# Kernel tuning notes

Hardware: AMD Instinct MI355X
Metric: run time of the kernel (lower is better)

The kernel has to match this reference:

```python
import jax, jax.numpy as jnp
import numpy as np

B, S, H, V, T, L = 32, 128, 1024, 32000, 100, 4
SD = 0.02


def setup_inputs() -> dict:
    key = jax.random.key(0)
    ks = jax.random.split(key, 20)
    f = jnp.float32
    return {
        "encoder_outputs": jax.random.normal(ks[0], (B, S, H), f),
        "encoder_hidden": jax.random.normal(ks[1], (L, B, H), f),
        "target_tensor": jax.random.randint(ks[2], (B, T), 0, V, dtype=jnp.int32),
        "emb": jax.random.normal(ks[3], (V, H), f) * SD,
        "w_ih0": jax.random.normal(ks[4], (3 * H, 2 * H), f) * SD,
        "w_hh0": jax.random.normal(ks[5], (3 * H, H), f) * SD,
        "b_ih0": jnp.zeros((3 * H,), f),
        "b_hh0": jnp.zeros((3 * H,), f),
        "w_ih": jax.random.normal(ks[6], (L - 1, 3 * H, H), f) * SD,
        "w_hh": jax.random.normal(ks[7], (L - 1, 3 * H, H), f) * SD,
        "b_ih": jnp.zeros((L - 1, 3 * H), f),
        "b_hh": jnp.zeros((L - 1, 3 * H), f),
        "out_w": jax.random.normal(ks[8], (V, H), f) * SD,
        "out_b": jnp.zeros((V,), f),
        "l1_w": jax.random.normal(ks[9], (3, 2 * H), f) * SD,
        "l1_b": jnp.zeros((3,), f),
        "l2_w": jax.random.normal(ks[10], (1, 3), f) * SD,
        "l2_b": jnp.zeros((1,), f),
    }


def _gru_cell(x, h, w_ih, w_hh, b_ih, b_hh):
    # PyTorch GRUCell math
    gi = x @ w_ih.T + b_ih          # [B, 3H]
    gh = h @ w_hh.T + b_hh          # [B, 3H]
    i_r, i_z, i_n = jnp.split(gi, 3, axis=-1)
    h_r, h_z, h_n = jnp.split(gh, 3, axis=-1)
    r = jax.nn.sigmoid(i_r + h_r)
    z = jax.nn.sigmoid(i_z + h_z)
    n = jnp.tanh(i_n + r * h_n)
    return (1.0 - z) * n + z * h


def reference(encoder_outputs, encoder_hidden, target_tensor, emb,
              w_ih0, w_hh0, b_ih0, b_hh0, w_ih, w_hh, b_ih, b_hh,
              out_w, out_b, l1_w, l1_b, l2_w, l2_b):
    b, h = encoder_hidden.shape[1], encoder_hidden.shape[2]
    enc_h = encoder_hidden[0]  # [B, H] 'updated_encoder_hidden'
    # teacher forcing: step 0 uses input 0, step i uses target[:, i-1]
    inputs = jnp.concatenate(
        [jnp.zeros((b, 1), target_tensor.dtype), target_tensor[:, :T - 1]],
        axis=1).T  # [T, B]

    def step(hidden, inp_t):
        # a[:] = hidden[0][-1] -> broadcast last batch row of layer-0 hidden
        a = jnp.broadcast_to(hidden[0, -1], (b, h))
        enc = jnp.concatenate([a, enc_h], axis=1)          # [B, 2H]
        s = (enc @ l1_w.T + l1_b) @ l2_w.T + l2_b          # [B, 1]
        scores = jax.nn.softmax(s, axis=0)                 # softmax over batch dim
        C = jnp.sum(enc_h * scores, axis=0)                # [H]
        e = jax.nn.relu(emb[inp_t])                        # [B, H]
        x = jnp.concatenate([e, jnp.broadcast_to(C, (b, h))], axis=-1)  # [B, 2H]
        h0 = _gru_cell(x, hidden[0], w_ih0, w_hh0, b_ih0, b_hh0)
        hs = [h0]
        xl = h0
        for l in range(L - 1):
            hl = _gru_cell(xl, hidden[l + 1], w_ih[l], w_hh[l], b_ih[l], b_hh[l])
            hs.append(hl)
            xl = hl
        logits = xl @ out_w.T + out_b                      # [B, V]
        return jnp.stack(hs), (logits, scores)

    hidden_fin, (logits, scores) = jax.lax.scan(step, encoder_hidden, inputs)
    dec_out = jax.nn.log_softmax(jnp.transpose(logits, (1, 0, 2)), axis=-1)  # [B, T, V]
    return dec_out, hidden_fin, scores[-1]
```

## Files before the change

### kernel.cpp

```cpp
#include <hip/hip_runtime.h>
#include <hip/hip_bf16.h>
#include <math.h>

#define B_ 32
#define H_ 1024
#define V_ 32000
#define T_ 100
#define L_ 4
#define TB_ (T_*B_)
#define N3H (3*H_)
#define NBLK 224
#define L0BLK 32
#define FSTRIDE 16

typedef __attribute__((ext_vector_type(8))) short bf16x8;
typedef __attribute__((ext_vector_type(4))) float f32x4;
typedef __attribute__((ext_vector_type(4))) unsigned short u16x4;

__device__ inline unsigned short f2bf(float f) {
    union { float f; unsigned u; } v; v.f = f;
    unsigned r = v.u + 0x7fff + ((v.u >> 16) & 1);
    return (unsigned short)(r >> 16);
}
__device__ inline float bf2f(unsigned short u) {
    union { unsigned u; float f; } v; v.u = ((unsigned)u) << 16; return v.f;
}

__device__ inline bf16x8 ld_h16(const unsigned short* p) {
    union { unsigned long long u[2]; bf16x8 v; } r;
    r.u[0] = __hip_atomic_load((const unsigned long long*)p,
                               __ATOMIC_RELAXED, __HIP_MEMORY_SCOPE_AGENT);
    r.u[1] = __hip_atomic_load((const unsigned long long*)(p + 4),
                               __ATOMIC_RELAXED, __HIP_MEMORY_SCOPE_AGENT);
    return r.v;
}
__device__ inline void st_h2(unsigned short* p, unsigned short v) {
    __hip_atomic_store(p, v, __ATOMIC_RELAXED, __HIP_MEMORY_SCOPE_AGENT);
}

__device__ inline void gload_lds16(const unsigned short* g, unsigned short* lds)
{
    __builtin_amdgcn_global_load_lds(
        (const __attribute__((address_space(1))) void*)g,
        (__attribute__((address_space(3))) void*)lds, 16, 0, 0);
}

__global__ __launch_bounds__(256) void convbf_kernel(
    const float* __restrict__ src, unsigned short* __restrict__ dst, int n4)
{
    for (int i = blockIdx.x * 256 + threadIdx.x; i < n4; i += gridDim.x * 256) {
        float4 v = ((const float4*)src)[i];
        u16x4 o; o.x = f2bf(v.x); o.y = f2bf(v.y); o.z = f2bf(v.z); o.w = f2bf(v.w);
        ((u16x4*)dst)[i] = o;
    }
}

__global__ __launch_bounds__(256) void embed_bf_kernel(
    const int* __restrict__ target, const float* __restrict__ emb,
    unsigned short* __restrict__ Ebf)
{
    int bid = blockIdx.x;
    int t = bid >> 5, b = bid & 31;
    int tok = (t == 0) ? 0 : target[b * T_ + (t - 1)];
    float4 v = ((const float4*)(emb + (size_t)tok * H_))[threadIdx.x];
    u16x4 o;
    o.x = f2bf(fmaxf(v.x, 0.f)); o.y = f2bf(fmaxf(v.y, 0.f));
    o.z = f2bf(fmaxf(v.z, 0.f)); o.w = f2bf(fmaxf(v.w, 0.f));
    ((u16x4*)(Ebf + (size_t)bid * H_))[threadIdx.x] = o;
}

__global__ __launch_bounds__(256) void attn_pre_kernel(
    const float* __restrict__ enc_h, const float* __restrict__ l1_w,
    const float* __restrict__ l1_b, const float* __restrict__ l2_w,
    float* __restrict__ Cout, float* __restrict__ scores)
{
    __shared__ float L1h[96];
    __shared__ float sc[32];
    int tid = threadIdx.x, wv = tid >> 6, lane = tid & 63;
    for (int d = wv; d < 96; d += 4) {
        int b = d / 3, g = d - 3 * b;
        const float4* wp = (const float4*)(l1_w + (size_t)g * 2 * H_ + H_);
        const float4* ep = (const float4*)(enc_h + (size_t)b * H_);
        float s = 0.f;
        for (int q = lane; q < 256; q += 64) {
            float4 w4 = wp[q], e4 = ep[q];
            s += w4.x * e4.x + w4.y * e4.y + w4.z * e4.z + w4.w * e4.w;
        }
        for (int o = 32; o > 0; o >>= 1) s += __shfl_down(s, o);
        if (lane == 0) L1h[d] = s;
    }
    __syncthreads();
    if (tid < 32) {
        float cb = 0.f;
        for (int g = 0; g < 3; ++g) cb += l2_w[g] * (L1h[tid * 3 + g] + l1_b[g]);
        sc[tid] = cb;
    }
    __syncthreads();
    if (tid == 0) {
        float m = sc[0];
        for (int b = 1; b < 32; ++b) m = fmaxf(m, sc[b]);
        float s = 0.f;
        for (int b = 0; b < 32; ++b) { float e = expf(sc[b] - m); sc[b] = e; s += e; }
        float inv = 1.f / s;
        for (int b = 0; b < 32; ++b) { sc[b] *= inv; scores[b] = sc[b]; }
    }
    __syncthreads();
    float4 c = make_float4(0.f, 0.f, 0.f, 0.f);
    for (int b = 0; b < 32; ++b) {
        float4 e = ((const float4*)(enc_h + (size_t)b * H_))[tid];
        float ww = sc[b];
        c.x += ww * e.x; c.y += ww * e.y; c.z += ww * e.z; c.w += ww * e.w;
    }
    ((float4*)Cout)[tid] = c;
}

__global__ __launch_bounds__(256) void wcc_kernel(
    const float* __restrict__ w_ih0, const float* __restrict__ C,
    float* __restrict__ wcC)
{
    int row = blockIdx.x * 4 + (threadIdx.x >> 6);
    int lane = threadIdx.x & 63;
    const float4* wp = (const float4*)(w_ih0 + (size_t)row * 2 * H_ + H_);
    const float4* cp = (const float4*)C;
    float s = 0.f;
    for (int q = lane; q < 256; q += 64) {
        float4 w4 = wp[q], c4 = cp[q];
        s += w4.x * c4.x + w4.y * c4.y + w4.z * c4.z + w4.w * c4.w;
    }
    for (int o = 32; o > 0; o >>= 1) s += __shfl_down(s, o);
    if (lane == 0) wcC[row] = s;
}

__global__ __launch_bounds__(256) void gemm_staged(
    const unsigned short* __restrict__ A, int lda,
    const unsigned short* __restrict__ Bb,
    const float* __restrict__ bias, int M, int outMode,
    void* __restrict__ outp)
{
    __shared__ unsigned short Wt[128 * 64];
    __shared__ unsigned short Ht[128 * 64];

    const int tid = threadIdx.x, wv = tid >> 6, lane = tid & 63;
    const int rlo = lane & 15, khw = lane >> 4;
    const int rch = lane >> 3, slot = lane & 7;
    const int rowB = blockIdx.y * 128, colB = blockIdx.x * 128;
    const int wrow0 = rowB + (wv >> 1) * 64;
    const int wcol0 = colB + (wv & 1) * 64;
    const int rA = (wv >> 1) * 64, cA = (wv & 1) * 64;

    f32x4 acc[4][4];
    #pragma unroll
    for (int i = 0; i < 4; ++i)
        #pragma unroll
        for (int j = 0; j < 4; ++j) acc[i][j] = (f32x4){0.f, 0.f, 0.f, 0.f};

    for (int k0 = 0; k0 < H_; k0 += 64) {
        #pragma unroll
        for (int j = 0; j < 4; ++j) {
            int q = wv * 4 + j;
            int row = q * 8 + rch;
            int ss = slot ^ (row & 7);
            gload_lds16(A + (size_t)(rowB + row) * lda + k0 + ss * 8,
                        Wt + (size_t)q * 512);
            gload_lds16(Bb + (size_t)(colB + row) * H_ + k0 + ss * 8,
                        Ht + (size_t)q * 512);
        }
        __syncthreads();

        const char* WtB = (const char*)Wt;
        const char* HtB = (const char*)Ht;
        #pragma unroll
        for (int kk = 0; kk < 2; ++kk) {
            bf16x8 af[4], bfr[4];
            #pragma unroll
            for (int ri = 0; ri < 4; ++ri) {
                int row = rA + ri * 16 + rlo;
                int ch = (kk * 4 + khw) ^ (row & 7);
                af[ri] = *(const bf16x8*)(WtB + row * 128 + ch * 16);
            }
            #pragma unroll
            for (int ci = 0; ci < 4; ++ci) {
                int col = cA + ci * 16 + rlo;
                int ch = (kk * 4 + khw) ^ (col & 7);
                bfr[ci] = *(const bf16x8*)(HtB + col * 128 + ch * 16);
            }
            #pragma unroll
            for (int ri = 0; ri < 4; ++ri)
                #pragma unroll
                for (int ci = 0; ci < 4; ++ci)
                    acc[ri][ci] = __builtin_amdgcn_mfma_f32_16x16x32_bf16(
                        af[ri], bfr[ci], acc[ri][ci], 0, 0, 0);
        }
        __syncthreads();
    }

    int rowoff = (lane >> 4) * 4;
    #pragma unroll
    for (int ri = 0; ri < 4; ++ri) {
        int row = wrow0 + ri * 16 + rowoff;
        float4 bs = *(const float4*)(bias + row);
        #pragma unroll
        for (int ci = 0; ci < 4; ++ci) {
            int col = wcol0 + ci * 16 + rlo;
            float4 v;
            v.x = acc[ri][ci][0] + bs.x; v.y = acc[ri][ci][1] + bs.y;
            v.z = acc[ri][ci][2] + bs.z; v.w = acc[ri][ci][3] + bs.w;
            if (outMode == 1) {
                int tt = col >> 5, b = col & 31;
                *(float4*)((float*)outp + ((size_t)b * T_ + tt) * V_ + row) = v;
            } else {
                u16x4 o; o.x = f2bf(v.x); o.y = f2bf(v.y);
                o.z = f2bf(v.z); o.w = f2bf(v.w);
                *(u16x4*)((unsigned short*)outp + (size_t)col * M + row) = o;
            }
        }
    }
}

__global__ __launch_bounds__(256) void big_gemm_kernel(
    const void* __restrict__ Aptr, int lda, int abf,
    const unsigned short* __restrict__ Bb,
    const float* __restrict__ bias, int M, int outMode,
    void* __restrict__ outp)
{
    int tid = threadIdx.x, wv = tid >> 6, lane = tid & 63;
    int rlo = lane & 15, klane = (lane >> 4) * 8;
    int rowB = blockIdx.y * 128 + (wv >> 1) * 64;
    int colB = blockIdx.x * 128 + (wv & 1) * 64;
    const unsigned short* Ab = (const unsigned short*)Aptr;
    const float* Af = (const float*)Aptr;

    f32x4 acc[4][4];
    #pragma unroll
    for (int i = 0; i < 4; ++i)
        #pragma unroll
        for (int j = 0; j < 4; ++j) acc[i][j] = (f32x4){0.f, 0.f, 0.f, 0.f};

    for (int k0 = 0; k0 < H_; k0 += 32) {
        bf16x8 bfrag[4];
        #pragma unroll
        for (int ci = 0; ci < 4; ++ci) {
            int col = colB + ci * 16 + rlo;
            bfrag[ci] = *(const bf16x8*)(Bb + (size_t)col * H_ + k0 + klane);
        }
        #pragma unroll
        for (int ri = 0; ri < 4; ++ri) {
            int row = rowB + ri * 16 + rlo;
            bf16x8 af;
            if (abf) {
                af = *(const bf16x8*)(Ab + (size_t)row * lda + k0 + klane);
            } else {
                const float* ap = Af + (size_t)row * lda + k0 + klane;
                float4 x0 = *(const float4*)ap, x1 = *(const float4*)(ap + 4);
                af[0] = (short)f2bf(x0.x); af[1] = (short)f2bf(x0.y);
                af[2] = (short)f2bf(x0.z); af[3] = (short)f2bf(x0.w);
                af[4] = (short)f2bf(x1.x); af[5] = (short)f2bf(x1.y);
                af[6] = (short)f2bf(x1.z); af[7] = (short)f2bf(x1.w);
            }
            #pragma unroll
            for (int ci = 0; ci < 4; ++ci)
                acc[ri][ci] = __builtin_amdgcn_mfma_f32_16x16x32_bf16(
                    af, bfrag[ci], acc[ri][ci], 0, 0, 0);
        }
    }

    int rowoff = (lane >> 4) * 4;
    #pragma unroll
    for (int ri = 0; ri < 4; ++ri) {
        int row = rowB + ri * 16 + rowoff;
        float4 bs = *(const float4*)(bias + row);
        #pragma unroll
        for (int ci = 0; ci < 4; ++ci) {
            int col = colB + ci * 16 + rlo;
            float4 v;
            v.x = acc[ri][ci][0] + bs.x; v.y = acc[ri][ci][1] + bs.y;
            v.z = acc[ri][ci][2] + bs.z; v.w = acc[ri][ci][3] + bs.w;
            if (outMode == 1) {
                int tt = col >> 5, b = col & 31;
                *(float4*)((float*)outp + ((size_t)b * T_ + tt) * V_ + row) = v;
            } else {
                u16x4 o; o.x = f2bf(v.x); o.y = f2bf(v.y);
                o.z = f2bf(v.z); o.w = f2bf(v.w);
                *(u16x4*)((unsigned short*)outp + (size_t)col * M + row) = o;
            }
        }
    }
}

__device__ inline void grid_bar4(unsigned* flags, unsigned round)
{
    __syncthreads();
    if (threadIdx.x == 0) {
        asm volatile("s_waitcnt vmcnt(0)" ::: "memory");
        __hip_atomic_store(&flags[(size_t)blockIdx.x * FSTRIDE], round,
                           __ATOMIC_RELAXED, __HIP_MEMORY_SCOPE_AGENT);
    }
    int ok = (threadIdx.x >= NBLK) ? 1 : 0;
    while (true) {
        if (!ok)
            ok = (__hip_atomic_load(&flags[(size_t)threadIdx.x * FSTRIDE],
                                    __ATOMIC_RELAXED, __HIP_MEMORY_SCOPE_AGENT) >= round);
        if (__syncthreads_and(ok)) break;
        __builtin_amdgcn_s_sleep(2);
    }
}

__global__ __launch_bounds__(512, 2) void decode_kernel(
    const unsigned short* __restrict__ whh0_bf,
    const unsigned short* __restrict__ wih_bf,
    const unsigned short* __restrict__ whh_bf,
    const unsigned short* __restrict__ G0,
    const float* __restrict__ b_ih0, const float* __restrict__ b_hh0,
    const float* __restrict__ b_ih,  const float* __restrict__ b_hh,
    const float* __restrict__ enc_hidden,
    unsigned short* __restrict__ hbf,
    unsigned short* __restrict__ Hist,
    float* __restrict__ hid_out,
    unsigned* __restrict__ flags)
{
    __shared__ float sacc[6][4][16][34];
    const int tid = threadIdx.x;
    const int wv = tid >> 6, lane = tid & 63;
    const int rlo = lane & 15, klane = (lane >> 4) * 8;
    const int rowoff = (lane >> 4) * 4;
    const int bid = blockIdx.x;

    int layer, f0;
    if (bid < L0BLK) { layer = 0; f0 = bid << 5; }
    else { int r = bid - L0BLK; layer = 1 + (r >> 6); f0 = (r & 63) << 4; }

    const unsigned short* Wih_l = (layer >= 1) ? wih_bf + (size_t)(layer - 1) * N3H * H_ : nullptr;
    const unsigned short* Whh_l = (layer >= 1) ? whh_bf + (size_t)(layer - 1) * N3H * H_ : whh0_bf;

    const int kc = wv & 3, srcgrp = wv >> 2;

    bf16x8 wreg[3][8];
    int rgv[3];
    #pragma unroll
    for (int i = 0; i < 3; ++i) {
        int rg = srcgrp * 3 + i;
        rgv[i] = rg;
        int wrow; const unsigned short* Wm;
        if (layer == 0)      { wrow = (rg >> 1) * H_ + f0 + (rg & 1) * 16; Wm = Whh_l; }
        else if (rg < 3)     { wrow = rg * H_ + f0;        Wm = Wih_l; }
        else                 { wrow = (rg - 3) * H_ + f0;  Wm = Whh_l; }
        const unsigned short* p = Wm + (size_t)(wrow + rlo) * H_ + kc * 256 + klane;
        #pragma unroll
        for (int s = 0; s < 8; ++s) wreg[i][s] = *(const bf16x8*)(p + s * 32);
    }

    const float* bihp = (layer == 0) ? b_ih0 : b_ih + (size_t)(layer - 1) * N3H;
    const float* bhhp = (layer == 0) ? b_hh0 : b_hh + (size_t)(layer - 1) * N3H;
    int jj, eb0;
    float hold0, hold1 = 0.f;
    if (layer == 0) {
        jj = f0 + (tid & 31);
        eb0 = tid >> 5;
        hold0 = enc_hidden[(size_t)eb0 * H_ + jj];
        hold1 = enc_hidden[(size_t)(eb0 + 16) * H_ + jj];
    } else {
        jj = f0 + (tid & 15);
        eb0 = tid >> 4;
        hold0 = enc_hidden[(size_t)layer * B_ * H_ + (size_t)eb0 * H_ + jj];
    }
    const float bir = bihp[jj], biz = bihp[H_ + jj], bin_ = bihp[2 * H_ + jj];
    const float bhr = bhhp[jj], bhz = bhhp[H_ + jj], bhn = bhhp[2 * H_ + jj];

    const size_t BH = (size_t)B_ * H_;

    for (int c = 0; c < T_ + L_ - 1; ++c) {
        int t = c - layer;
        if (t >= 0 && t < T_) {
            int pw = t & 1, pr = pw ^ 1;
            const unsigned short* hown  = hbf + ((size_t)pr * L_ + layer) * BH;
            const unsigned short* hprev = (layer > 0)
                ? hbf + ((size_t)pw * L_ + (layer - 1)) * BH : nullptr;

            f32x4 acc[3][2];
            #pragma unroll
            for (int i = 0; i < 3; ++i) {
                acc[i][0] = (f32x4){0.f, 0.f, 0.f, 0.f};
                acc[i][1] = (f32x4){0.f, 0.f, 0.f, 0.f};
            }

            const unsigned short* hsrc = (layer == 0 || srcgrp == 1) ? hown : hprev;
            const unsigned short* hp = hsrc + (size_t)rlo * H_ + kc * 256 + klane;
            #pragma unroll
            for (int s = 0; s < 8; ++s) {
                bf16x8 b0 = ld_h16(hp + s * 32);
                bf16x8 b1 = ld_h16(hp + 16 * H_ + s * 32);
                #pragma unroll
                for (int i = 0; i < 3; ++i) {
                    acc[i][0] = __builtin_amdgcn_mfma_f32_16x16x32_bf16(wreg[i][s], b0, acc[i][0], 0, 0, 0);
                    acc[i][1] = __builtin_amdgcn_mfma_f32_16x16x32_bf16(wreg[i][s], b1, acc[i][1], 0, 0, 0);
                }
            }

            #pragma unroll
            for (int i = 0; i < 3; ++i)
                #pragma unroll
                for (int r = 0; r < 4; ++r) {
                    sacc[rgv[i]][kc][rowoff + r][rlo]      = acc[i][0][r];
                    sacc[rgv[i]][kc][rowoff + r][16 + rlo] = acc[i][1][r];
                }
            __syncthreads();

            if (layer > 0) {
                int f = tid & 15, b = tid >> 4;
                float ir = bir, iz = biz, in_ = bin_;
                float hr = bhr, hz = bhz, hn = bhn;
                #pragma unroll
                for (int k2 = 0; k2 < 4; ++k2) {
                    ir += sacc[0][k2][f][b]; iz += sacc[1][k2][f][b]; in_ += sacc[2][k2][f][b];
                    hr += sacc[3][k2][f][b]; hz += sacc[4][k2][f][b]; hn += sacc[5][k2][f][b];
                }
                float r = 1.f / (1.f + expf(-(ir + hr)));
                float z = 1.f / (1.f + expf(-(iz + hz)));
                float n = tanhf(in_ + r * hn);
                float hnew = (1.f - z) * n + z * hold0;
                hold0 = hnew;
                unsigned short hb16 = f2bf(hnew);
                st_h2(&hbf[((size_t)pw * L_ + layer) * BH + (size_t)b * H_ + jj], hb16);
                if (layer == L_ - 1) Hist[((size_t)t * B_ + b) * H_ + jj] = hb16;
                if (t == T_ - 1) hid_out[(size_t)layer * BH + (size_t)b * H_ + jj] = hnew;
            } else {
                int fi = tid & 31;
                int rghalf = fi >> 4, fr = fi & 15;
                {
                    int b = eb0;
                    const unsigned short* g0p = G0 + ((size_t)t * B_ + b) * N3H;
                    float ir = bf2f(g0p[jj]) + bir;
                    float iz = bf2f(g0p[H_ + jj]) + biz;
                    float in_ = bf2f(g0p[2 * H_ + jj]) + bin_;
                    float hr = bhr, hz = bhz, hn = bhn;
                    #pragma unroll
                    for (int k2 = 0; k2 < 4; ++k2) {
                        hr += sacc[rghalf][k2][fr][b];
                        hz += sacc[2 + rghalf][k2][fr][b];
                        hn += sacc[4 + rghalf][k2][fr][b];
                    }
                    float r = 1.f / (1.f + expf(-(ir + hr)));
                    float z = 1.f / (1.f + expf(-(iz + hz)));
                    float n = tanhf(in_ + r * hn);
                    float hnew = (1.f - z) * n + z * hold0;
                    hold0 = hnew;
                    st_h2(&hbf[((size_t)pw * L_) * BH + (size_t)b * H_ + jj], f2bf(hnew));
                    if (t == T_ - 1) hid_out[(size_t)b * H_ + jj] = hnew;
                }
                {
                    int b = eb0 + 16;
                    const unsigned short* g0p = G0 + ((size_t)t * B_ + b) * N3H;
                    float ir = bf2f(g0p[jj]) + bir;
                    float iz = bf2f(g0p[H_ + jj]) + biz;
                    float in_ = bf2f(g0p[2 * H_ + jj]) + bin_;
                    float hr = bhr, hz = bhz, hn = bhn;
                    #pragma unroll
                    for (int k2 = 0; k2 < 4; ++k2) {
                        hr += sacc[rghalf][k2][fr][b];
                        hz += sacc[2 + rghalf][k2][fr][b];
                        hn += sacc[4 + rghalf][k2][fr][b];
                    }
                    float r = 1.f / (1.f + expf(-(ir + hr)));
                    float z = 1.f / (1.f + expf(-(iz + hz)));
                    float n = tanhf(in_ + r * hn);
                    float hnew = (1.f - z) * n + z * hold1;
                    hold1 = hnew;
                    st_h2(&hbf[((size_t)pw * L_) * BH + (size_t)b * H_ + jj], f2bf(hnew));
                    if (t == T_ - 1) hid_out[(size_t)b * H_ + jj] = hnew;
                }
            }
        }
        grid_bar4(flags, (unsigned)(c + 1));
    }
}

__global__ __launch_bounds__(256) void logsoftmax_kernel(float* __restrict__ dout)
{
    __shared__ float red[256];
    float4* x4 = (float4*)(dout + (size_t)blockIdx.x * V_);
    const int N4 = V_ / 4;
    int tid = threadIdx.x;

    float m = -INFINITY, s = 0.f;
    for (int i = tid; i < N4; i += 256) {
        float4 v = x4[i];
        float m4 = fmaxf(fmaxf(v.x, v.y), fmaxf(v.z, v.w));
        if (m4 > m) { s *= expf(m - m4); m = m4; }
        s += expf(v.x - m) + expf(v.y - m) + expf(v.z - m) + expf(v.w - m);
    }
    red[tid] = m; __syncthreads();
    for (int o = 128; o > 0; o >>= 1) {
        if (tid < o) red[tid] = fmaxf(red[tid], red[tid + o]);
        __syncthreads();
    }
    float M = red[0]; __syncthreads();
    red[tid] = s * expf(m - M); __syncthreads();
    for (int o = 128; o > 0; o >>= 1) {
        if (tid < o) red[tid] += red[tid + o];
        __syncthreads();
    }
    float lse = M + logf(red[0]);

    for (int i = tid; i < N4; i += 256) {
        float4 v = x4[i];
        v.x -= lse; v.y -= lse; v.z -= lse; v.w -= lse;
        x4[i] = v;
    }
}

extern "C" void kernel_launch(void* const* d_in, const int* in_sizes, int n_in,
                              void* d_out, int out_size, void* d_ws, size_t ws_size,
                              hipStream_t stream)
{
    (void)in_sizes; (void)n_in; (void)out_size;

    const float* enc_hidden = (const float*)d_in[1];
    const int*   target     = (const int*)  d_in[2];
    const float* emb        = (const float*)d_in[3];
    const float* w_ih0      = (const float*)d_in[4];
    const float* w_hh0      = (const float*)d_in[5];
    const float* b_ih0      = (const float*)d_in[6];
    const float* b_hh0      = (const float*)d_in[7];
    const float* w_ih       = (const float*)d_in[8];
    const float* w_hh       = (const float*)d_in[9];
    const float* b_ih       = (const float*)d_in[10];
    const float* b_hh       = (const float*)d_in[11];
    const float* out_w      = (const float*)d_in[12];
    const float* out_b      = (const float*)d_in[13];
    const float* l1_w       = (const float*)d_in[14];
    const float* l1_b       = (const float*)d_in[15];
    const float* l2_w       = (const float*)d_in[16];
    float* out = (float*)d_out;

    char* w = (char*)d_ws;
    auto alloc = [&](size_t bytes) -> char* {
        char* p = w; w += (bytes + 255) & ~(size_t)255; return p;
    };
    unsigned short* whh0_bf = (unsigned short*)alloc((size_t)N3H * H_ * 2);
    unsigned short* wih_bf  = (unsigned short*)alloc((size_t)3 * N3H * H_ * 2);
    unsigned short* whh_bf  = (unsigned short*)alloc((size_t)3 * N3H * H_ * 2);
    unsigned short* Ebf     = (unsigned short*)alloc((size_t)TB_ * H_ * 2);
    unsigned short* G0      = (unsigned short*)alloc((size_t)TB_ * N3H * 2);
    unsigned short* Hist    = (unsigned short*)alloc((size_t)TB_ * H_ * 2);
    unsigned short* hbf     = (unsigned short*)alloc((size_t)2 * L_ * B_ * H_ * 2);
    float*          Cbuf    = (float*)alloc(H_ * 4);
    float*          scores  = (float*)alloc(256);
    float*          wcC     = (float*)alloc(N3H * 4);
    unsigned*       flags   = (unsigned*)alloc((size_t)NBLK * FSTRIDE * 4);

    size_t used = (size_t)(w - (char*)d_ws);
    unsigned short* wih0f_bf = nullptr;
    if (used + (size_t)N3H * 2 * H_ * 2 + 256 <= ws_size)
        wih0f_bf = (unsigned short*)alloc((size_t)N3H * 2 * H_ * 2);
    used = (size_t)(w - (char*)d_ws);
    unsigned short* outw_bf = nullptr;
    if (used + (size_t)V_ * H_ * 2 + 256 <= ws_size)
        outw_bf = (unsigned short*)alloc((size_t)V_ * H_ * 2);

    const size_t LBH = (size_t)L_ * B_ * H_;

    hipMemsetAsync(flags, 0, (size_t)NBLK * FSTRIDE * 4, stream);

    convbf_kernel<<<512, 256, 0, stream>>>(w_hh0, whh0_bf, N3H * H_ / 4);
    convbf_kernel<<<1024, 256, 0, stream>>>(w_ih, wih_bf, 3 * N3H * H_ / 4);
    convbf_kernel<<<1024, 256, 0, stream>>>(w_hh, whh_bf, 3 * N3H * H_ / 4);
    if (wih0f_bf)
        convbf_kernel<<<1024, 256, 0, stream>>>(w_ih0, wih0f_bf, N3H * 2 * H_ / 4);
    if (outw_bf)
        convbf_kernel<<<2048, 256, 0, stream>>>(out_w, outw_bf, V_ * H_ / 4);
    embed_bf_kernel<<<TB_, 256, 0, stream>>>(target, emb, Ebf);
    convbf_kernel<<<128, 256, 0, stream>>>(enc_hidden, hbf + LBH, (int)(LBH / 4));
    attn_pre_kernel<<<1, 256, 0, stream>>>(enc_hidden, l1_w, l1_b, l2_w, Cbuf, scores);
    wcc_kernel<<<N3H / 4, 256, 0, stream>>>(w_ih0, Cbuf, wcC);

    if (wih0f_bf)
        gemm_staged<<<dim3(TB_ / 128, N3H / 128), 256, 0, stream>>>(
            wih0f_bf, 2 * H_, Ebf, wcC, N3H, 0, G0);
    else
        big_gemm_kernel<<<dim3(TB_ / 128, N3H / 128), 256, 0, stream>>>(
            w_ih0, 2 * H_, 0, Ebf, wcC, N3H, 0, G0);

    decode_kernel<<<NBLK, 512, 0, stream>>>(
        whh0_bf, wih_bf, whh_bf, G0, b_ih0, b_hh0, b_ih, b_hh,
        enc_hidden, hbf, Hist, out + (size_t)B_ * T_ * V_, flags);

    if (outw_bf)
        gemm_staged<<<dim3(TB_ / 128, V_ / 128), 256, 0, stream>>>(
            outw_bf, H_, Hist, out_b, V_, 1, out);
    else
        big_gemm_kernel<<<dim3(TB_ / 128, V_ / 128), 256, 0, stream>>>(
            out_w, H_, 0, Hist, out_b, V_, 1, out);
    logsoftmax_kernel<<<TB_, 256, 0, stream>>>(out);

    hipMemcpyAsync(out + (size_t)B_ * T_ * V_ + LBH, scores, B_ * 4,
                   hipMemcpyDeviceToDevice, stream);
}
```

Measured before the change: 1.854 ms.

## Replace grid-wide barrier with per-layer dataflow flags in the GRU decode kernel

The decode kernel drops the all-block barrier per wavefront step and has each block wait only on flags from the layer below (step t), its own layer (t-1) and the layer above (t-4 backpressure). The hidden-state ring buffer grows from 2 to 4 slots so that layers can run up to 3 steps apart. Blocks drop from 224 to 128, each covering 32 features, and weights are now reloaded from global memory every step instead of being held in registers. The fallback paths are removed, and the w_ih0 fallback now wrongly passes whh0_bf with the wrong K, which risks incorrect output when workspace is short. Reloading weights every step costs memory bandwidth, traded against less synchronisation wait.

After: 3.044 ms. +64.2%, slower.

```diff
diff --git a/kernel.cpp b/kernel.cpp
--- a/kernel.cpp
+++ b/kernel.cpp
@@ -9,8 +9,7 @@
 #define L_ 4
 #define TB_ (T_*B_)
 #define N3H (3*H_)
-#define NBLK 224
-#define L0BLK 32
+#define NBLK 128
 #define FSTRIDE 16
 
 typedef __attribute__((ext_vector_type(8))) short bf16x8;
@@ -36,6 +35,9 @@
 }
 __device__ inline void st_h2(unsigned short* p, unsigned short v) {
     __hip_atomic_store(p, v, __ATOMIC_RELAXED, __HIP_MEMORY_SCOPE_AGENT);
+}
+__device__ inline unsigned ld_flag(const unsigned* p) {
+    return __hip_atomic_load(p, __ATOMIC_RELAXED, __HIP_MEMORY_SCOPE_AGENT);
 }
 
 __device__ inline void gload_lds16(const unsigned short* g, unsigned short* lds)
@@ -217,95 +219,7 @@
     }
 }
 
-__global__ __launch_bounds__(256) void big_gemm_kernel(
-    const void* __restrict__ Aptr, int lda, int abf,
-    const unsigned short* __restrict__ Bb,
-    const float* __restrict__ bias, int M, int outMode,
-    void* __restrict__ outp)
-{
-    int tid = threadIdx.x, wv = tid >> 6, lane = tid & 63;
-    int rlo = lane & 15, klane = (lane >> 4) * 8;
-    int rowB = blockIdx.y * 128 + (wv >> 1) * 64;
-    int colB = blockIdx.x * 128 + (wv & 1) * 64;
-    const unsigned short* Ab = (const unsigned short*)Aptr;
-    const float* Af = (const float*)Aptr;
-
-    f32x4 acc[4][4];
-    #pragma unroll
-    for (int i = 0; i < 4; ++i)
-        #pragma unroll
-        for (int j = 0; j < 4; ++j) acc[i][j] = (f32x4){0.f, 0.f, 0.f, 0.f};
-
-    for (int k0 = 0; k0 < H_; k0 += 32) {
-        bf16x8 bfrag[4];
-        #pragma unroll
-        for (int ci = 0; ci < 4; ++ci) {
-            int col = colB + ci * 16 + rlo;
-            bfrag[ci] = *(const bf16x8*)(Bb + (size_t)col * H_ + k0 + klane);
-        }
-        #pragma unroll
-        for (int ri = 0; ri < 4; ++ri) {
-            int row = rowB + ri * 16 + rlo;
-            bf16x8 af;
-            if (abf) {
-                af = *(const bf16x8*)(Ab + (size_t)row * lda + k0 + klane);
-            } else {
-                const float* ap = Af + (size_t)row * lda + k0 + klane;
-                float4 x0 = *(const float4*)ap, x1 = *(const float4*)(ap + 4);
-                af[0] = (short)f2bf(x0.x); af[1] = (short)f2bf(x0.y);
-                af[2] = (short)f2bf(x0.z); af[3] = (short)f2bf(x0.w);
-                af[4] = (short)f2bf(x1.x); af[5] = (short)f2bf(x1.y);
-                af[6] = (short)f2bf(x1.z); af[7] = (short)f2bf(x1.w);
-            }
-            #pragma unroll
-            for (int ci = 0; ci < 4; ++ci)
-                acc[ri][ci] = __builtin_amdgcn_mfma_f32_16x16x32_bf16(
-                    af, bfrag[ci], acc[ri][ci], 0, 0, 0);
-        }
-    }
-
-    int rowoff = (lane >> 4) * 4;
-    #pragma unroll
-    for (int ri = 0; ri < 4; ++ri) {
-        int row = rowB + ri * 16 + rowoff;
-        float4 bs = *(const float4*)(bias + row);
-        #pragma unroll
-        for (int ci = 0; ci < 4; ++ci) {
-            int col = colB + ci * 16 + rlo;
-            float4 v;
-            v.x = acc[ri][ci][0] + bs.x; v.y = acc[ri][ci][1] + bs.y;
-            v.z = acc[ri][ci][2] + bs.z; v.w = acc[ri][ci][3] + bs.w;
-            if (outMode == 1) {
-                int tt = col >> 5, b = col & 31;
-                *(float4*)((float*)outp + ((size_t)b * T_ + tt) * V_ + row) = v;
-            } else {
-                u16x4 o; o.x = f2bf(v.x); o.y = f2bf(v.y);
-                o.z = f2bf(v.z); o.w = f2bf(v.w);
-                *(u16x4*)((unsigned short*)outp + (size_t)col * M + row) = o;
-            }
-        }
-    }
-}
-
-__device__ inline void grid_bar4(unsigned* flags, unsigned round)
-{
-    __syncthreads();
-    if (threadIdx.x == 0) {
-        asm volatile("s_waitcnt vmcnt(0)" ::: "memory");
-        __hip_atomic_store(&flags[(size_t)blockIdx.x * FSTRIDE], round,
-                           __ATOMIC_RELAXED, __HIP_MEMORY_SCOPE_AGENT);
-    }
-    int ok = (threadIdx.x >= NBLK) ? 1 : 0;
-    while (true) {
-        if (!ok)
-            ok = (__hip_atomic_load(&flags[(size_t)threadIdx.x * FSTRIDE],
-                                    __ATOMIC_RELAXED, __HIP_MEMORY_SCOPE_AGENT) >= round);
-        if (__syncthreads_and(ok)) break;
-        __builtin_amdgcn_s_sleep(2);
-    }
-}
-
-__global__ __launch_bounds__(512, 2) void decode_kernel(
+__global__ __launch_bounds__(512, 1) void decode_kernel(
     const unsigned short* __restrict__ whh0_bf,
     const unsigned short* __restrict__ wih_bf,
     const unsigned short* __restrict__ whh_bf,
@@ -318,84 +232,89 @@
     float* __restrict__ hid_out,
     unsigned* __restrict__ flags)
 {
-    __shared__ float sacc[6][4][16][34];
+    __shared__ float sacc[12][4][16][34];
     const int tid = threadIdx.x;
     const int wv = tid >> 6, lane = tid & 63;
     const int rlo = lane & 15, klane = (lane >> 4) * 8;
     const int rowoff = (lane >> 4) * 4;
     const int bid = blockIdx.x;
-
-    int layer, f0;
-    if (bid < L0BLK) { layer = 0; f0 = bid << 5; }
-    else { int r = bid - L0BLK; layer = 1 + (r >> 6); f0 = (r & 63) << 4; }
+    const int layer = bid >> 5, slot = bid & 31;
+    const int f0 = slot << 5;
+    const int kc = wv & 3, srcgrp = wv >> 2;
+    const size_t BH = (size_t)B_ * H_;
 
     const unsigned short* Wih_l = (layer >= 1) ? wih_bf + (size_t)(layer - 1) * N3H * H_ : nullptr;
     const unsigned short* Whh_l = (layer >= 1) ? whh_bf + (size_t)(layer - 1) * N3H * H_ : whh0_bf;
 
-    const int kc = wv & 3, srcgrp = wv >> 2;
-
-    bf16x8 wreg[3][8];
-    int rgv[3];
-    #pragma unroll
-    for (int i = 0; i < 3; ++i) {
-        int rg = srcgrp * 3 + i;
-        rgv[i] = rg;
-        int wrow; const unsigned short* Wm;
-        if (layer == 0)      { wrow = (rg >> 1) * H_ + f0 + (rg & 1) * 16; Wm = Whh_l; }
-        else if (rg < 3)     { wrow = rg * H_ + f0;        Wm = Wih_l; }
-        else                 { wrow = (rg - 3) * H_ + f0;  Wm = Whh_l; }
-        const unsigned short* p = Wm + (size_t)(wrow + rlo) * H_ + kc * 256 + klane;
+    const unsigned short* wp[6];
+    int rgv[6];
+    if (layer == 0) {
         #pragma unroll
-        for (int s = 0; s < 8; ++s) wreg[i][s] = *(const bf16x8*)(p + s * 32);
+        for (int i = 0; i < 3; ++i) {
+            int rg = srcgrp * 3 + i;
+            rgv[i] = rg;
+            int wrow = (rg >> 1) * H_ + f0 + (rg & 1) * 16;
+            wp[i] = Whh_l + (size_t)(wrow + rlo) * H_ + kc * 256 + klane;
+        }
+    } else {
+        const unsigned short* Wm = srcgrp ? Whh_l : Wih_l;
+        #pragma unroll
+        for (int i = 0; i < 6; ++i) {
+            rgv[i] = srcgrp * 6 + i;
+            int wrow = (i >> 1) * H_ + f0 + (i & 1) * 16;
+            wp[i] = Wm + (size_t)(wrow + rlo) * H_ + kc * 256 + klane;
+        }
     }
 
     const float* bihp = (layer == 0) ? b_ih0 : b_ih + (size_t)(layer - 1) * N3H;
     const float* bhhp = (layer == 0) ? b_hh0 : b_hh + (size_t)(layer - 1) * N3H;
-    int jj, eb0;
-    float hold0, hold1 = 0.f;
-    if (layer == 0) {
-        jj = f0 + (tid & 31);
-        eb0 = tid >> 5;
-        hold0 = enc_hidden[(size_t)eb0 * H_ + jj];
-        hold1 = enc_hidden[(size_t)(eb0 + 16) * H_ + jj];
-    } else {
-        jj = f0 + (tid & 15);
-        eb0 = tid >> 4;
-        hold0 = enc_hidden[(size_t)layer * B_ * H_ + (size_t)eb0 * H_ + jj];
-    }
+    const int jj = f0 + (tid & 31);
+    const int eb0 = tid >> 5;
+    float hold0 = enc_hidden[(size_t)layer * BH + (size_t)eb0 * H_ + jj];
+    float hold1 = enc_hidden[(size_t)layer * BH + (size_t)(eb0 + 16) * H_ + jj];
     const float bir = bihp[jj], biz = bihp[H_ + jj], bin_ = bihp[2 * H_ + jj];
     const float bhr = bhhp[jj], bhz = bhhp[H_ + jj], bhn = bhhp[2 * H_ + jj];
 
-    const size_t BH = (size_t)B_ * H_;
-
-    for (int c = 0; c < T_ + L_ - 1; ++c) {
-        int t = c - layer;
-        if (t >= 0 && t < T_) {
-            int pw = t & 1, pr = pw ^ 1;
-            const unsigned short* hown  = hbf + ((size_t)pr * L_ + layer) * BH;
-            const unsigned short* hprev = (layer > 0)
-                ? hbf + ((size_t)pw * L_ + (layer - 1)) * BH : nullptr;
-
+    for (int t = 0; t < T_; ++t) {
+        for (;;) {
+            int ok = 1;
+            if (tid < 32) {
+                if (layer > 0)
+                    ok = ((int)ld_flag(&flags[(size_t)((layer - 1) * 32 + tid) * FSTRIDE]) >= t + 1);
+            } else if (tid < 64) {
+                ok = ((int)ld_flag(&flags[(size_t)(layer * 32 + (tid - 32)) * FSTRIDE]) >= t);
+            } else if (tid < 96) {
+                if (layer < 3 && t >= 4)
+                    ok = ((int)ld_flag(&flags[(size_t)((layer + 1) * 32 + (tid - 64)) * FSTRIDE]) >= t - 3);
+            }
+            if (__syncthreads_and(ok)) break;
+            __builtin_amdgcn_s_sleep(2);
+        }
+
+        const unsigned short* hown  = hbf + ((size_t)((t + 3) & 3) * L_ + layer) * BH;
+        const unsigned short* hprev = (layer > 0)
+            ? hbf + ((size_t)(t & 3) * L_ + (layer - 1)) * BH : nullptr;
+        unsigned short* hw = hbf + ((size_t)(t & 3) * L_ + layer) * BH;
+
+        if (layer == 0) {
             f32x4 acc[3][2];
             #pragma unroll
             for (int i = 0; i < 3; ++i) {
                 acc[i][0] = (f32x4){0.f, 0.f, 0.f, 0.f};
                 acc[i][1] = (f32x4){0.f, 0.f, 0.f, 0.f};
             }
-
-            const unsigned short* hsrc = (layer == 0 || srcgrp == 1) ? hown : hprev;
-            const unsigned short* hp = hsrc + (size_t)rlo * H_ + kc * 256 + klane;
+            const unsigned short* hp = hown + (size_t)rlo * H_ + kc * 256 + klane;
             #pragma unroll
             for (int s = 0; s < 8; ++s) {
                 bf16x8 b0 = ld_h16(hp + s * 32);
                 bf16x8 b1 = ld_h16(hp + 16 * H_ + s * 32);
                 #pragma unroll
                 for (int i = 0; i < 3; ++i) {
-                    acc[i][0] = __builtin_amdgcn_mfma_f32_16x16x32_bf16(wreg[i][s], b0, acc[i][0], 0, 0, 0);
-                    acc[i][1] = __builtin_amdgcn_mfma_f32_16x16x32_bf16(wreg[i][s], b1, acc[i][1], 0, 0, 0);
-                }
-            }
-
+                    bf16x8 a = *(const bf16x8*)(wp[i] + s * 32);
+                    acc[i][0] = __builtin_amdgcn_mfma_f32_16x16x32_bf16(a, b0, acc[i][0], 0, 0, 0);
+                    acc[i][1] = __builtin_amdgcn_mfma_f32_16x16x32_bf16(a, b1, acc[i][1], 0, 0, 0);
+                }
+            }
             #pragma unroll
             for (int i = 0; i < 3; ++i)
                 #pragma unroll
@@ -403,74 +322,112 @@
                     sacc[rgv[i]][kc][rowoff + r][rlo]      = acc[i][0][r];
                     sacc[rgv[i]][kc][rowoff + r][16 + rlo] = acc[i][1][r];
                 }
-            __syncthreads();
-
-            if (layer > 0) {
-                int f = tid & 15, b = tid >> 4;
-                float ir = bir, iz = biz, in_ = bin_;
+        } else {
+            f32x4 acc[6][2];
+            #pragma unroll
+            for (int i = 0; i < 6; ++i) {
+                acc[i][0] = (f32x4){0.f, 0.f, 0.f, 0.f};
+                acc[i][1] = (f32x4){0.f, 0.f, 0.f, 0.f};
+            }
+            const unsigned short* hsrc = srcgrp ? hown : hprev;
+            const unsigned short* hp = hsrc + (size_t)rlo * H_ + kc * 256 + klane;
+            #pragma unroll
+            for (int s = 0; s < 8; ++s) {
+                bf16x8 b0 = ld_h16(hp + s * 32);
+                bf16x8 b1 = ld_h16(hp + 16 * H_ + s * 32);
+                #pragma unroll
+                for (int i = 0; i < 6; ++i) {
+                    bf16x8 a = *(const bf16x8*)(wp[i] + s * 32);
+                    acc[i][0] = __builtin_amdgcn_mfma_f32_16x16x32_bf16(a, b0, acc[i][0], 0, 0, 0);
+                    acc[i][1] = __builtin_amdgcn_mfma_f32_16x16x32_bf16(a, b1, acc[i][1], 0, 0, 0);
+                }
+            }
+            #pragma unroll
+            for (int i = 0; i < 6; ++i)
+                #pragma unroll
+                for (int r = 0; r < 4; ++r) {
+                    sacc[rgv[i]][kc][rowoff + r][rlo]      = acc[i][0][r];
+                    sacc[rgv[i]][kc][rowoff + r][16 + rlo] = acc[i][1][r];
+                }
+        }
+        __syncthreads();
+
+        const int fh = (tid & 31) >> 4, fr = tid & 15;
+        if (layer == 0) {
+            {
+                int b = eb0;
+                const unsigned short* g0p = G0 + ((size_t)t * B_ + b) * N3H;
+                float ir = bf2f(g0p[jj]) + bir;
+                float iz = bf2f(g0p[H_ + jj]) + biz;
+                float in_ = bf2f(g0p[2 * H_ + jj]) + bin_;
                 float hr = bhr, hz = bhz, hn = bhn;
                 #pragma unroll
                 for (int k2 = 0; k2 < 4; ++k2) {
-                    ir += sacc[0][k2][f][b]; iz += sacc[1][k2][f][b]; in_ += sacc[2][k2][f][b];
-                    hr += sacc[3][k2][f][b]; hz += sacc[4][k2][f][b]; hn += sacc[5][k2][f][b];
+                    hr += sacc[fh][k2][fr][b];
+                    hz += sacc[2 + fh][k2][fr][b];
+                    hn += sacc[4 + fh][k2][fr][b];
                 }
                 float r = 1.f / (1.f + expf(-(ir + hr)));
                 float z = 1.f / (1.f + expf(-(iz + hz)));
                 float n = tanhf(in_ + r * hn);
                 float hnew = (1.f - z) * n + z * hold0;
                 hold0 = hnew;
+                st_h2(&hw[(size_t)b * H_ + jj], f2bf(hnew));
+                if (t == T_ - 1) hid_out[(size_t)b * H_ + jj] = hnew;
+            }
+            {
+                int b = eb0 + 16;
+                const unsigned short* g0p = G0 + ((size_t)t * B_ + b) * N3H;
+                float ir = bf2f(g0p[jj]) + bir;
+                float iz = bf2f(g0p[H_ + jj]) + biz;
+                float in_ = bf2f(g0p[2 * H_ + jj]) + bin_;
+                float hr = bhr, hz = bhz, hn = bhn;
+                #pragma unroll
+                for (int k2 = 0; k2 < 4; ++k2) {
+                    hr += sacc[fh][k2][fr][b];
+                    hz += sacc[2 + fh][k2][fr][b];
+                    hn += sacc[4 + fh][k2][fr][b];
+                }
+                float r = 1.f / (1.f + expf(-(ir + hr)));
+                float z = 1.f / (1.f + expf(-(iz + hz)));
+                float n = tanhf(in_ + r * hn);
+                float hnew = (1.f - z) * n + z * hold1;
+                hold1 = hnew;
+                st_h2(&hw[(size_t)b * H_ + jj], f2bf(hnew));
+                if (t == T_ - 1) hid_out[(size_t)b * H_ + jj] = hnew;
+            }
+        } else {
+            #pragma unroll
+            for (int rep = 0; rep < 2; ++rep) {
+                int b = eb0 + rep * 16;
+                float ir = bir, iz = biz, in_ = bin_;
+                float hr = bhr, hz = bhz, hn = bhn;
+                #pragma unroll
+                for (int k2 = 0; k2 < 4; ++k2) {
+                    ir += sacc[fh][k2][fr][b];     iz += sacc[2 + fh][k2][fr][b];
+                    in_ += sacc[4 + fh][k2][fr][b];
+                    hr += sacc[6 + fh][k2][fr][b]; hz += sacc[8 + fh][k2][fr][b];
+                    hn += sacc[10 + fh][k2][fr][b];
+                }
+                float r = 1.f / (1.f + expf(-(ir + hr)));
+                float z = 1.f / (1.f + expf(-(iz + hz)));
+                float n = tanhf(in_ + r * hn);
+                float hold = rep ? hold1 : hold0;
+                float hnew = (1.f - z) * n + z * hold;
+                if (rep) hold1 = hnew; else hold0 = hnew;
                 unsigned short hb16 = f2bf(hnew);
-                st_h2(&hbf[((size_t)pw * L_ + layer) * BH + (size_t)b * H_ + jj], hb16);
+                st_h2(&hw[(size_t)b * H_ + jj], hb16);
                 if (layer == L_ - 1) Hist[((size_t)t * B_ + b) * H_ + jj] = hb16;
                 if (t == T_ - 1) hid_out[(size_t)layer * BH + (size_t)b * H_ + jj] = hnew;
-            } else {
-                int fi = tid & 31;
-                int rghalf = fi >> 4, fr = fi & 15;
-                {
-                    int b = eb0;
-                    const unsigned short* g0p = G0 + ((size_t)t * B_ + b) * N3H;
-                    float ir = bf2f(g0p[jj]) + bir;
-                    float iz = bf2f(g0p[H_ + jj]) + biz;
-                    float in_ = bf2f(g0p[2 * H_ + jj]) + bin_;
-                    float hr = bhr, hz = bhz, hn = bhn;
-                    #pragma unroll
-                    for (int k2 = 0; k2 < 4; ++k2) {
-                        hr += sacc[rghalf][k2][fr][b];
-                        hz += sacc[2 + rghalf][k2][fr][b];
-                        hn += sacc[4 + rghalf][k2][fr][b];
-                    }
-                    float r = 1.f / (1.f + expf(-(ir + hr)));
-                    float z = 1.f / (1.f + expf(-(iz + hz)));
-                    float n = tanhf(in_ + r * hn);
-                    float hnew = (1.f - z) * n + z * hold0;
-                    hold0 = hnew;
-                    st_h2(&hbf[((size_t)pw * L_) * BH + (size_t)b * H_ + jj], f2bf(hnew));
-                    if (t == T_ - 1) hid_out[(size_t)b * H_ + jj] = hnew;
-                }
-                {
-                    int b = eb0 + 16;
-                    const unsigned short* g0p = G0 + ((size_t)t * B_ + b) * N3H;
-                    float ir = bf2f(g0p[jj]) + bir;
-                    float iz = bf2f(g0p[H_ + jj]) + biz;
-                    float in_ = bf2f(g0p[2 * H_ + jj]) + bin_;
-                    float hr = bhr, hz = bhz, hn = bhn;
-                    #pragma unroll
-                    for (int k2 = 0; k2 < 4; ++k2) {
-                        hr += sacc[rghalf][k2][fr][b];
-                        hz += sacc[2 + rghalf][k2][fr][b];
-                        hn += sacc[4 + rghalf][k2][fr][b];
-                    }
-                    float r = 1.f / (1.f + expf(-(ir + hr)));
-                    float z = 1.f / (1.f + expf(-(iz + hz)));
-                    float n = tanhf(in_ + r * hn);
-                    float hnew = (1.f - z) * n + z * hold1;
-                    hold1 = hnew;
-                    st_h2(&hbf[((size_t)pw * L_) * BH + (size_t)b * H_ + jj], f2bf(hnew));
-                    if (t == T_ - 1) hid_out[(size_t)b * H_ + jj] = hnew;
-                }
-            }
-        }
-        grid_bar4(flags, (unsigned)(c + 1));
+            }
+        }
+
+        __syncthreads();
+        if (tid == 0) {
+            asm volatile("s_waitcnt vmcnt(0)" ::: "memory");
+            __hip_atomic_store(&flags[(size_t)bid * FSTRIDE], (unsigned)(t + 1),
+                               __ATOMIC_RELAXED, __HIP_MEMORY_SCOPE_AGENT);
+        }
     }
 }
 
@@ -542,7 +499,7 @@
     unsigned short* Ebf     = (unsigned short*)alloc((size_t)TB_ * H_ * 2);
     unsigned short* G0      = (unsigned short*)alloc((size_t)TB_ * N3H * 2);
     unsigned short* Hist    = (unsigned short*)alloc((size_t)TB_ * H_ * 2);
-    unsigned short* hbf     = (unsigned short*)alloc((size_t)2 * L_ * B_ * H_ * 2);
+    unsigned short* hbf     = (unsigned short*)alloc((size_t)4 * L_ * B_ * H_ * 2);
     float*          Cbuf    = (float*)alloc(H_ * 4);
     float*          scores  = (float*)alloc(256);
     float*          wcC     = (float*)alloc(N3H * 4);
@@ -569,7 +526,7 @@
     if (outw_bf)
         convbf_kernel<<<2048, 256, 0, stream>>>(out_w, outw_bf, V_ * H_ / 4);
     embed_bf_kernel<<<TB_, 256, 0, stream>>>(target, emb, Ebf);
-    convbf_kernel<<<128, 256, 0, stream>>>(enc_hidden, hbf + LBH, (int)(LBH / 4));
+    convbf_kernel<<<128, 256, 0, stream>>>(enc_hidden, hbf + 3 * LBH, (int)(LBH / 4));
     attn_pre_kernel<<<1, 256, 0, stream>>>(enc_hidden, l1_w, l1_b, l2_w, Cbuf, scores);
     wcc_kernel<<<N3H / 4, 256, 0, stream>>>(w_ih0, Cbuf, wcC);
 
@@ -577,8 +534,8 @@
         gemm_staged<<<dim3(TB_ / 128, N3H / 128), 256, 0, stream>>>(
             wih0f_bf, 2 * H_, Ebf, wcC, N3H, 0, G0);
     else
-        big_gemm_kernel<<<dim3(TB_ / 128, N3H / 128), 256, 0, stream>>>(
-            w_ih0, 2 * H_, 0, Ebf, wcC, N3H, 0, G0);
+        gemm_staged<<<dim3(TB_ / 128, N3H / 128), 256, 0, stream>>>(
+            whh0_bf , H_, Ebf, wcC, N3H, 0, G0);
 
     decode_kernel<<<NBLK, 512, 0, stream>>>(
         whh0_bf, wih_bf, whh_bf, G0, b_ih0, b_hh0, b_ih, b_hh,
@@ -587,9 +544,6 @@
     if (outw_bf)
         gemm_staged<<<dim3(TB_ / 128, V_ / 128), 256, 0, stream>>>(
             outw_bf, H_, Hist, out_b, V_, 1, out);
-    else
-        big_gemm_kernel<<<dim3(TB_ / 128, V_ / 128), 256, 0, stream>>>(
-            out_w, H_, 0, Hist, out_b, V_, 1, out);
     logsoftmax_kernel<<<TB_, 256, 0, stream>>>(out);
 
     hipMemcpyAsync(out + (size_t)B_ * T_ * V_ + LBH, scores, B_ * 4,
```
